# Optimization experiments

Hardware: AMD Instinct MI355X
Metric: run time of the kernel (lower is better)

The kernel has to match this reference:

```python
import jax, jax.numpy as jnp
import numpy as np
import math

L, HEADS, K, NFFN, H = 4, 8, 32, 2, 256  # layers, attention heads, top-k neighbors, FFN layers, hidden


def mish(x):
    return x * jnp.tanh(jax.nn.softplus(x))


def layernorm(x, a, b, eps=1e-6):
    # torch LayerNorm-style with UNBIASED std (x.std default), matching the source
    mean = x.mean(-1, keepdims=True)
    var = jnp.sum((x - mean) ** 2, axis=-1, keepdims=True) / (x.shape[-1] - 1)
    return a * (x - mean) / (jnp.sqrt(var) + eps) + b


def linear(x, W, b):
    # torch nn.Linear: y = x @ W^T + b, W is [out, in]
    return jnp.einsum('...i,oi->...o', x, W) + b


def setup_inputs() -> dict:
    key = jax.random.key(0)
    ks = jax.random.split(key, 6)
    node_features = jax.random.normal(ks[0], (16, 512, H), dtype=jnp.float32)
    edge_features = jax.random.uniform(ks[1], (16, 512, 512), dtype=jnp.float32)
    masks = jnp.ones((16, 512), dtype=jnp.int32)
    attn_W = jax.random.normal(ks[2], (L, 4, H, H), dtype=jnp.float32) * 0.05  # q,k,v,out per layer
    attn_b = jnp.zeros((L, 4, H), dtype=jnp.float32)
    ffn_W = jax.random.normal(ks[3], (L, NFFN, H, H), dtype=jnp.float32) * 0.05
    ffn_b = jnp.zeros((L, NFFN, H), dtype=jnp.float32)
    ln_a = jnp.ones((H,), dtype=jnp.float32)
    ln_b = jnp.zeros((H,), dtype=jnp.float32)
    return {"node_features": node_features, "edge_features": edge_features, "masks": masks,
            "attn_W": attn_W, "attn_b": attn_b, "ffn_W": ffn_W, "ffn_b": ffn_b,
            "ln_a": ln_a, "ln_b": ln_b}


def reference(node_features, edge_features, masks, attn_W, attn_b, ffn_W, ffn_b, ln_a, ln_b):
    b, m, _ = node_features.shape
    d = H // HEADS
    scale = 1.0 / math.sqrt(d)

    # top-k edge-weight mask (double argsort rank trick, as in source); deterministic
    rank = jnp.argsort(jnp.argsort(-edge_features, axis=-1), axis=-1)
    ew = edge_features * (rank < K)
    ew = ew / (jnp.sum(ew, axis=-1, keepdims=True) + 1e-5)  # [b, m, m]

    col_mask = (masks == 0)[:, None, None, :]  # broadcast over heads and query rows

    x = node_features
    for i in range(L):
        x = layernorm(x, ln_a, ln_b)
        # MHSA
        def split_heads(y):
            return y.reshape(b, m, HEADS, d).transpose(0, 2, 1, 3)  # b h m d
        q = split_heads(linear(x, attn_W[i, 0], attn_b[i, 0]))
        k = split_heads(linear(x, attn_W[i, 1], attn_b[i, 1]))
        v = split_heads(linear(x, attn_W[i, 2], attn_b[i, 2]))
        scores = jnp.einsum('bhmd,bhnd->bhmn', q, k)
        scores = jnp.where(col_mask, -1e12, scores)
        scores = jax.nn.softmax(scores * ew[:, None] * scale, axis=-1)
        attn_out = jnp.einsum('bhmn,bhnd->bhmd', scores, v)
        attn_out = attn_out.transpose(0, 2, 1, 3).reshape(b, m, H)
        attn_out = mish(linear(attn_out, attn_W[i, 3], attn_b[i, 3]))
        x = x + attn_out
        x = layernorm(x, ln_a, ln_b)
        # FFN: all layers use mish (output_act_fn='mish')
        y = x
        for j in range(NFFN):
            y = mish(linear(y, ffn_W[i, j], ffn_b[i, j]))
        x = x + y
    return x
```

## Files before the change

### kernel.cpp

```cpp
#include <hip/hip_runtime.h>
#include <cstddef>

#define NB 16
#define NM 512
#define NHID 256
#define NTOPK 32
#define NROWS (NB*NM)
#define NLAYER 4

typedef unsigned short ushort_t;
typedef __attribute__((ext_vector_type(8))) short short8;
typedef __attribute__((ext_vector_type(4))) short short4v;
typedef __attribute__((ext_vector_type(4))) float f32x4;

#define FRAG_OFF(row, c8) (((c8) >> 2) * 1024 + ((((c8) & 3) << 4) + (((row) & 15) ^ ((c8) >> 2))) * 16)
#define FRAG_RD(ks, lane) ((ks) * 1024 + ((((lane) >> 4) << 4) + (((lane) & 15) ^ (ks))) * 16)

#define MFMA16(a, b, c) __builtin_amdgcn_mfma_f32_16x16x32_bf16((a), (b), (c), 0, 0, 0)

__device__ __forceinline__ float mish_f(float v) {
    if (v > 20.0f) return v;
    float t = __expf(v);
    float u = t * (t + 2.0f);
    return v * (u / (u + 2.0f));
}
__device__ __forceinline__ ushort_t f2b(float f) {
    unsigned u = __float_as_uint(f);
    return (ushort_t)((u + 0x7FFFu + ((u >> 16) & 1u)) >> 16);
}
__device__ __forceinline__ float b2f(ushort_t h) {
    return __uint_as_float(((unsigned)h) << 16);
}

__global__ __launch_bounds__(256) void prep_kernel(const float* __restrict__ edge,
                                                   int* __restrict__ tidx,
                                                   float* __restrict__ tw,
                                                   const float* __restrict__ attnW,
                                                   const float* __restrict__ ffnW,
                                                   ushort_t* __restrict__ wb) {
    if (blockIdx.x < 768) {
        int t = blockIdx.x * 256 + threadIdx.x;
        int frag = t >> 9, r = t & 511;
        int ks = r >> 6, l = r & 63;
        const float* src;
        if (frag < 256) src = attnW + ((size_t)(frag >> 6) * 1024 + (frag & 63) * 16 + (l & 15)) * 256;
        else { int fi = frag - 256; src = ffnW + ((size_t)(fi >> 5) * 512 + (fi & 31) * 16 + (l & 15)) * 256; }
        src += ks * 32 + (l >> 4) * 8;
        short8 o;
        #pragma unroll
        for (int j = 0; j < 8; ++j) o[j] = (short)f2b(src[j]);
        *(short8*)(wb + (size_t)t * 8) = o;
        return;
    }
    const int lane = threadIdx.x & 63, w = threadIdx.x >> 6;
    const int row = (blockIdx.x - 768) * 4 + w;
    const float* er = edge + (size_t)row * NM;
    float v[8]; unsigned u[8];
    #pragma unroll
    for (int s = 0; s < 8; ++s) { v[s] = er[s * 64 + lane]; u[s] = __float_as_uint(v[s]); }
    unsigned T = 0;
    for (int bit = 31; bit >= 0; --bit) {
        unsigned Tc = T | (1u << bit);
        int c = 0;
        #pragma unroll
        for (int s = 0; s < 8; ++s) c += (int)__popcll(__ballot(u[s] >= Tc));
        if (c >= NTOPK) T = Tc;
    }
    int cgt = 0;
    #pragma unroll
    for (int s = 0; s < 8; ++s) cgt += (int)__popcll(__ballot(u[s] > T));
    const int extra = NTOPK - cgt;
    float psum = 0.f;
    #pragma unroll
    for (int s = 0; s < 8; ++s) psum += (u[s] > T) ? v[s] : 0.f;
    psum += __shfl_xor(psum, 1); psum += __shfl_xor(psum, 2); psum += __shfl_xor(psum, 4);
    psum += __shfl_xor(psum, 8); psum += __shfl_xor(psum, 16); psum += __shfl_xor(psum, 32);
    const float ssum = psum + (float)extra * __uint_as_float(T);
    const float rden = 0.17677669529663687f / (ssum + 1e-5f);
    const unsigned long long lmask = (1ull << lane) - 1ull;
    int base = 0, eqbase = 0;
    #pragma unroll
    for (int s = 0; s < 8; ++s) {
        bool gt = (u[s] > T), eq = (u[s] == T);
        unsigned long long meq = __ballot(eq);
        int eqrank = eqbase + (int)__popcll(meq & lmask);
        bool sel = gt || (eq && eqrank < extra);
        unsigned long long msel = __ballot(sel);
        if (sel) {
            int pos = base + (int)__popcll(msel & lmask);
            tidx[row * NTOPK + pos] = s * 64 + lane;
            tw[row * NTOPK + pos] = v[s] * rden;
        }
        base += (int)__popcll(msel);
        eqbase += (int)__popcll(meq);
    }
}

__global__ __launch_bounds__(256) void k1_ln_qkv(const float* __restrict__ xin,
                                                 float* __restrict__ x,
                                                 float* __restrict__ q,
                                                 ushort_t* __restrict__ kvb,
                                                 float* __restrict__ part,
                                                 const ushort_t* __restrict__ wf,
                                                 const float* __restrict__ bias,
                                                 const float* __restrict__ ga,
                                                 const float* __restrict__ gb) {
    __shared__ __align__(16) char af[8192];
    const int tid = threadIdx.x, lane = tid & 63, w = tid >> 6;
    const int bx = blockIdx.x;
    const int wid = (bx & 7) * 64 + (bx >> 3);
    const int bm = wid * 16, bb = wid >> 5, blk = wid & 31;
    const int zb = blockIdx.y;
    {
        const int rr = lane >> 4, c16 = (lane & 15) << 4;
        const int ri = (w << 2) + rr;
        const float* xr = xin + (size_t)(bm + ri) * NHID + c16;
        f32x4 v0 = *(const f32x4*)(xr);
        f32x4 v1 = *(const f32x4*)(xr + 4);
        f32x4 v2 = *(const f32x4*)(xr + 8);
        f32x4 v3 = *(const f32x4*)(xr + 12);
        float s = 0.f;
        #pragma unroll
        for (int k = 0; k < 4; ++k) s += v0[k] + v1[k] + v2[k] + v3[k];
        s += __shfl_xor(s, 1); s += __shfl_xor(s, 2); s += __shfl_xor(s, 4); s += __shfl_xor(s, 8);
        float mean = s * (1.0f / NHID);
        float vr = 0.f;
        #pragma unroll
        for (int k = 0; k < 4; ++k) {
            float d0 = v0[k]-mean, d1 = v1[k]-mean, d2 = v2[k]-mean, d3 = v3[k]-mean;
            vr += d0*d0 + d1*d1 + d2*d2 + d3*d3;
        }
        vr += __shfl_xor(vr, 1); vr += __shfl_xor(vr, 2); vr += __shfl_xor(vr, 4); vr += __shfl_xor(vr, 8);
        vr *= (1.0f / (NHID - 1));
        float rs = 1.0f / (sqrtf(vr) + 1e-6f);
        f32x4 g0 = *(const f32x4*)(ga + c16), g1 = *(const f32x4*)(ga + c16 + 4);
        f32x4 g2 = *(const f32x4*)(ga + c16 + 8), g3 = *(const f32x4*)(ga + c16 + 12);
        f32x4 h0 = *(const f32x4*)(gb + c16), h1 = *(const f32x4*)(gb + c16 + 4);
        f32x4 h2 = *(const f32x4*)(gb + c16 + 8), h3 = *(const f32x4*)(gb + c16 + 12);
        f32x4 o0, o1, o2, o3;
        #pragma unroll
        for (int k = 0; k < 4; ++k) {
            o0[k] = g0[k]*(v0[k]-mean)*rs + h0[k];
            o1[k] = g1[k]*(v1[k]-mean)*rs + h1[k];
            o2[k] = g2[k]*(v2[k]-mean)*rs + h2[k];
            o3[k] = g3[k]*(v3[k]-mean)*rs + h3[k];
        }
        if (zb == 0) {
            float* xw = x + (size_t)(bm + ri) * NHID + c16;
            *(f32x4*)(xw) = o0; *(f32x4*)(xw + 4) = o1;
            *(f32x4*)(xw + 8) = o2; *(f32x4*)(xw + 12) = o3;
        }
        short8 p0, p1;
        #pragma unroll
        for (int k = 0; k < 4; ++k) {
            p0[k] = (short)f2b(o0[k]); p0[4+k] = (short)f2b(o1[k]);
            p1[k] = (short)f2b(o2[k]); p1[4+k] = (short)f2b(o3[k]);
        }
        int c8 = (lane & 15) * 2;
        *(short8*)(af + FRAG_OFF(ri, c8)) = p0;
        *(short8*)(af + FRAG_OFF(ri, c8 + 1)) = p1;
    }
    __syncthreads();
    short8 a[8];
    #pragma unroll
    for (int ks = 0; ks < 8; ++ks) a[ks] = *(const short8*)(af + FRAG_RD(ks, lane));
    #pragma unroll
    for (int gi = 0; gi < 3; ++gi) {
        const int col0 = (zb * 3 + gi) * 128 + w * 32;
        f32x4 acc0 = {}, acc1 = {};
        const ushort_t* bp0 = wf + ((size_t)((col0 >> 4) * 8) * 64 + lane) * 8;
        const ushort_t* bp1 = bp0 + 4096;
        #pragma unroll
        for (int ks = 0; ks < 8; ++ks) {
            short8 b0 = *(const short8*)(bp0 + ks * 512);
            short8 b1 = *(const short8*)(bp1 + ks * 512);
            acc0 = MFMA16(a[ks], b0, acc0);
            acc1 = MFMA16(a[ks], b1, acc1);
        }
        const int rbase = bm + (lane >> 4) * 4;
        #pragma unroll
        for (int ni = 0; ni < 2; ++ni) {
            int col = col0 + ni * 16 + (lane & 15);
            float bv = bias[col];
            f32x4 A = ni ? acc1 : acc0;
            #pragma unroll
            for (int j = 0; j < 4; ++j) {
                int row = rbase + j;
                float vv = A[j] + bv;
                if (col < 256) q[(size_t)row * 256 + col] = vv;
                else kvb[(size_t)row * 512 + (col - 256)] = f2b(vv);
            }
            if (zb == 1 && gi >= 1) {
                float s2 = A[0] + A[1] + A[2] + A[3] + 4.0f * bv;
                s2 += __shfl_xor(s2, 16); s2 += __shfl_xor(s2, 32);
                if (lane < 16)
                    part[((size_t)bb * 32 + blk) * 256 + (col0 + ni * 16 + lane - 512)] = s2;
            }
        }
    }
}

template<int LAST>
__global__ __launch_bounds__(1024, 4) void kb_layer(float* __restrict__ x,
                                                    float* __restrict__ q,
                                                    const ushort_t* __restrict__ kvb_cur,
                                                    ushort_t* __restrict__ kvb_nxt,
                                                    const float* __restrict__ part_cur,
                                                    float* __restrict__ part_nxt,
                                                    const int* __restrict__ tidx,
                                                    const float* __restrict__ tw,
                                                    const int* __restrict__ msk,
                                                    const ushort_t* __restrict__ wfo,
                                                    const ushort_t* __restrict__ wf1,
                                                    const ushort_t* __restrict__ wf2,
                                                    const ushort_t* __restrict__ wqn,
                                                    const float* __restrict__ bo,
                                                    const float* __restrict__ b1,
                                                    const float* __restrict__ b2,
                                                    const float* __restrict__ bqn,
                                                    const float* __restrict__ ga,
                                                    const float* __restrict__ gb) {
    __shared__ __align__(16) float regA[32 * 256];
    __shared__ __align__(16) char regB[16384];
    __shared__ __align__(16) char regC[16384];
    const int tid = threadIdx.x, lane = tid & 63, w = tid >> 6;
    const int wid = (blockIdx.x & 7) * 32 + (blockIdx.x >> 3);
    const int R0 = wid * 32, bb = wid >> 4, blk = wid & 15;
    int* sidx = (int*)regC;
    float* sws = (float*)(regC + 4096);
    float* vsumf = regA;
    {
        int nb = tidx[(size_t)R0 * NTOPK + tid];
        float wv = tw[(size_t)R0 * NTOPK + tid];
        sidx[tid] = (msk[bb * NM + nb] == 0) ? (nb | (int)0x80000000) : nb;
        sws[tid] = wv;
    }
    if (tid < 256) {
        float s = 0.f;
        #pragma unroll
        for (int p = 0; p < 32; ++p) s += part_cur[((size_t)bb * 32 + p) * 256 + tid];
        vsumf[tid] = s;
    }
    float xres[2][4];
    #pragma unroll
    for (int rh = 0; rh < 2; ++rh)
        #pragma unroll
        for (int j = 0; j < 4; ++j)
            xres[rh][j] = x[(size_t)(R0 + rh * 16 + (lane >> 4) * 4 + j) * NHID + w * 16 + (lane & 15)];
    const int rl = w * 2 + (lane >> 5);
    const int cbase = (lane & 31) * 8;
    float qv[8];
    {
        const float* qp = q + (size_t)(R0 + rl) * 256 + cbase;
        f32x4 q0 = *(const f32x4*)qp, q1 = *(const f32x4*)(qp + 4);
        #pragma unroll
        for (int k = 0; k < 4; ++k) { qv[k] = q0[k]; qv[4 + k] = q1[k]; }
    }
    __syncthreads();
    {
        float accv[8] = {};
        float den = 0.f;
        for (int j = 0; j < NTOPK; ++j) {
            int raw = sidx[rl * 32 + j];
            float swv = sws[rl * 32 + j];
            const ushort_t* kp = kvb_cur + ((size_t)(bb * NM + (raw & 511))) * 512 + cbase;
            short8 kA = *(const short8*)(kp);
            short8 vA = *(const short8*)(kp + 256);
            float p = 0.f;
            #pragma unroll
            for (int t = 0; t < 8; ++t) p += qv[t] * b2f((ushort_t)kA[t]);
            p += __shfl_xor(p, 1); p += __shfl_xor(p, 2);
            float sarg = (raw < 0) ? -1e12f : p;
            float e = __expf(sarg * swv);
            float em1 = e - 1.0f;
            den += em1;
            #pragma unroll
            for (int t = 0; t < 8; ++t) accv[t] += em1 * b2f((ushort_t)vA[t]);
        }
        float rden = 1.0f / (den + 512.0f);
        short8 p0;
        #pragma unroll
        for (int t = 0; t < 8; ++t) p0[t] = (short)f2b((accv[t] + vsumf[cbase + t]) * rden);
        *(short8*)(regB + (rl >> 4) * 8192 + FRAG_OFF(rl, (lane & 31))) = p0;
    }
    __syncthreads();
    {
        short8 b[8];
        const ushort_t* bp = wfo + ((size_t)(w * 8) * 64 + lane) * 8;
        #pragma unroll
        for (int ks = 0; ks < 8; ++ks) b[ks] = *(const short8*)(bp + ks * 512);
        int col = w * 16 + (lane & 15);
        float bv = bo[col];
        #pragma unroll
        for (int rh = 0; rh < 2; ++rh) {
            f32x4 acc = {};
            #pragma unroll
            for (int ks = 0; ks < 8; ++ks)
                acc = MFMA16(*(const short8*)(regB + rh * 8192 + FRAG_RD(ks, lane)), b[ks], acc);
            #pragma unroll
            for (int j = 0; j < 4; ++j) {
                int row = rh * 16 + (lane >> 4) * 4 + j;
                regA[row * 256 + col] = mish_f(acc[j] + bv) + xres[rh][j];
            }
        }
    }
    __syncthreads();
    {
        const int c0 = (lane & 31) * 8;
        float* xr = regA + rl * 256 + c0;
        f32x4 v0 = *(const f32x4*)xr, v1 = *(const f32x4*)(xr + 4);
        float s = v0[0]+v0[1]+v0[2]+v0[3]+v1[0]+v1[1]+v1[2]+v1[3];
        s += __shfl_xor(s,1); s += __shfl_xor(s,2); s += __shfl_xor(s,4);
        s += __shfl_xor(s,8); s += __shfl_xor(s,16);
        float mean = s * (1.0f / NHID);
        float vr = 0.f;
        #pragma unroll
        for (int k = 0; k < 4; ++k) {
            float d0 = v0[k]-mean, d1 = v1[k]-mean;
            vr += d0*d0 + d1*d1;
        }
        vr += __shfl_xor(vr,1); vr += __shfl_xor(vr,2); vr += __shfl_xor(vr,4);
        vr += __shfl_xor(vr,8); vr += __shfl_xor(vr,16);
        vr *= (1.0f / (NHID - 1));
        float rs = 1.0f / (sqrtf(vr) + 1e-6f);
        f32x4 g0 = *(const f32x4*)(ga + c0), g1 = *(const f32x4*)(ga + c0 + 4);
        f32x4 h0 = *(const f32x4*)(gb + c0), h1 = *(const f32x4*)(gb + c0 + 4);
        f32x4 o0, o1;
        #pragma unroll
        for (int k = 0; k < 4; ++k) {
            o0[k] = g0[k]*(v0[k]-mean)*rs + h0[k];
            o1[k] = g1[k]*(v1[k]-mean)*rs + h1[k];
        }
        *(f32x4*)xr = o0; *(f32x4*)(xr + 4) = o1;
        short8 p;
        #pragma unroll
        for (int k = 0; k < 4; ++k) { p[k] = (short)f2b(o0[k]); p[4+k] = (short)f2b(o1[k]); }
        *(short8*)(regB + (rl >> 4) * 8192 + FRAG_OFF(rl, (lane & 31))) = p;
    }
    __syncthreads();
    {
        short8 b[8];
        const ushort_t* bp = wf1 + ((size_t)(w * 8) * 64 + lane) * 8;
        #pragma unroll
        for (int ks = 0; ks < 8; ++ks) b[ks] = *(const short8*)(bp + ks * 512);
        int col = w * 16 + (lane & 15);
        float bv = b1[col];
        int c8 = col >> 3;
        #pragma unroll
        for (int rh = 0; rh < 2; ++rh) {
            f32x4 acc = {};
            #pragma unroll
            for (int ks = 0; ks < 8; ++ks)
                acc = MFMA16(*(const short8*)(regB + rh * 8192 + FRAG_RD(ks, lane)), b[ks], acc);
            #pragma unroll
            for (int j = 0; j < 4; ++j) {
                int row = rh * 16 + (lane >> 4) * 4 + j;
                *(ushort_t*)(regC + rh * 8192 + FRAG_OFF(row, c8) + (col & 7) * 2) = f2b(mish_f(acc[j] + bv));
            }
        }
    }
    __syncthreads();
    {
        short8 b[8];
        const ushort_t* bp = wf2 + ((size_t)(w * 8) * 64 + lane) * 8;
        #pragma unroll
        for (int ks = 0; ks < 8; ++ks) b[ks] = *(const short8*)(bp + ks * 512);
        int col = w * 16 + (lane & 15);
        float bv = b2[col];
        #pragma unroll
        for (int rh = 0; rh < 2; ++rh) {
            f32x4 acc = {};
            #pragma unroll
            for (int ks = 0; ks < 8; ++ks)
                acc = MFMA16(*(const short8*)(regC + rh * 8192 + FRAG_RD(ks, lane)), b[ks], acc);
            #pragma unroll
            for (int j = 0; j < 4; ++j) {
                int row = rh * 16 + (lane >> 4) * 4 + j;
                float v = mish_f(acc[j] + bv) + regA[row * 256 + col];
                if (LAST) x[(size_t)(R0 + row) * NHID + col] = v;
                else regA[row * 256 + col] = v;
            }
        }
    }
    if (LAST) return;
    __syncthreads();
    {
        const int c0 = (lane & 31) * 8;
        float* xr = regA + rl * 256 + c0;
        f32x4 v0 = *(const f32x4*)xr, v1 = *(const f32x4*)(xr + 4);
        float s = v0[0]+v0[1]+v0[2]+v0[3]+v1[0]+v1[1]+v1[2]+v1[3];
        s += __shfl_xor(s,1); s += __shfl_xor(s,2); s += __shfl_xor(s,4);
        s += __shfl_xor(s,8); s += __shfl_xor(s,16);
        float mean = s * (1.0f / NHID);
        float vr = 0.f;
        #pragma unroll
        for (int k = 0; k < 4; ++k) {
            float d0 = v0[k]-mean, d1 = v1[k]-mean;
            vr += d0*d0 + d1*d1;
        }
        vr += __shfl_xor(vr,1); vr += __shfl_xor(vr,2); vr += __shfl_xor(vr,4);
        vr += __shfl_xor(vr,8); vr += __shfl_xor(vr,16);
        vr *= (1.0f / (NHID - 1));
        float rs = 1.0f / (sqrtf(vr) + 1e-6f);
        f32x4 g0 = *(const f32x4*)(ga + c0), g1 = *(const f32x4*)(ga + c0 + 4);
        f32x4 h0 = *(const f32x4*)(gb + c0), h1 = *(const f32x4*)(gb + c0 + 4);
        f32x4 o0, o1;
        #pragma unroll
        for (int k = 0; k < 4; ++k) {
            o0[k] = g0[k]*(v0[k]-mean)*rs + h0[k];
            o1[k] = g1[k]*(v1[k]-mean)*rs + h1[k];
        }
        float* xg = x + (size_t)(R0 + rl) * NHID + c0;
        *(f32x4*)xg = o0; *(f32x4*)(xg + 4) = o1;
        short8 p;
        #pragma unroll
        for (int k = 0; k < 4; ++k) { p[k] = (short)f2b(o0[k]); p[4+k] = (short)f2b(o1[k]); }
        *(short8*)(regB + (rl >> 4) * 8192 + FRAG_OFF(rl, (lane & 31))) = p;
    }
    __syncthreads();
    {
        #pragma unroll
        for (int gg = 0; gg < 3; ++gg) {
            const int ct = w + gg * 16;
            short8 b[8];
            const ushort_t* bp = wqn + (size_t)ct * 4096 + (size_t)lane * 8;
            #pragma unroll
            for (int ks = 0; ks < 8; ++ks) b[ks] = *(const short8*)(bp + ks * 512);
            int col = ct * 16 + (lane & 15);
            float bv = bqn[col];
            #pragma unroll
            for (int rh = 0; rh < 2; ++rh) {
                f32x4 acc = {};
                #pragma unroll
                for (int ks = 0; ks < 8; ++ks)
                    acc = MFMA16(*(const short8*)(regB + rh * 8192 + FRAG_RD(ks, lane)), b[ks], acc);
                #pragma unroll
                for (int j = 0; j < 4; ++j) {
                    int row = rh * 16 + (lane >> 4) * 4 + j;
                    float vv = acc[j] + bv;
                    if (col < 256) q[(size_t)(R0 + row) * 256 + col] = vv;
                    else kvb_nxt[(size_t)(R0 + row) * 512 + (col - 256)] = f2b(vv);
                }
                if (gg == 2) {
                    float s2 = acc[0] + acc[1] + acc[2] + acc[3] + 4.0f * bv;
                    s2 += __shfl_xor(s2, 16); s2 += __shfl_xor(s2, 32);
                    if (lane < 16)
                        part_nxt[((size_t)bb * 32 + blk * 2 + rh) * 256 + (ct * 16 + lane - 512)] = s2;
                }
            }
        }
    }
}

extern "C" void kernel_launch(void* const* d_in, const int* in_sizes, int n_in,
                              void* d_out, int out_size, void* d_ws, size_t ws_size,
                              hipStream_t stream) {
    (void)in_sizes; (void)n_in; (void)out_size; (void)ws_size;
    const float* node  = (const float*)d_in[0];
    const float* edge  = (const float*)d_in[1];
    const int*   msk   = (const int*)d_in[2];
    const float* attnW = (const float*)d_in[3];
    const float* attnB = (const float*)d_in[4];
    const float* ffnW  = (const float*)d_in[5];
    const float* ffnB  = (const float*)d_in[6];
    const float* lna   = (const float*)d_in[7];
    const float* lnb   = (const float*)d_in[8];

    float* x = (float*)d_out;
    float* wsf = (float*)d_ws;
    float*    q     = wsf;
    ushort_t* kvbA  = (ushort_t*)(wsf + 2097152);
    ushort_t* kvbB  = (ushort_t*)(wsf + 4194304);
    ushort_t* wb    = (ushort_t*)(wsf + 6291456);
    float*    tw    = wsf + 7077888;
    int*      tidx  = (int*)(wsf + 7340032);
    float*    partA = wsf + 7602176;
    float*    partB = wsf + 7733248;

    prep_kernel<<<2816, 256, 0, stream>>>(edge, tidx, tw, attnW, ffnW, wb);
    k1_ln_qkv<<<dim3(512, 2), 256, 0, stream>>>(node, x, q, kvbA, partA,
                                                wb, attnB, lna, lnb);
    for (int l = 0; l < NLAYER; ++l) {
        ushort_t* kv_c = (l & 1) ? kvbB : kvbA;
        ushort_t* kv_n = (l & 1) ? kvbA : kvbB;
        float* pt_c = (l & 1) ? partB : partA;
        float* pt_n = (l & 1) ? partA : partB;
        const ushort_t* wfo = wb + (size_t)(l * 64 + 48) * 4096;
        const ushort_t* wf1 = wb + (size_t)(256 + l * 32) * 4096;
        const ushort_t* wf2 = wb + (size_t)(256 + l * 32 + 16) * 4096;
        const ushort_t* wqn = wb + (size_t)(((l + 1) & 3) * 64) * 4096;
        const float* bo  = attnB + (size_t)l * 1024 + 768;
        const float* b1  = ffnB + (size_t)l * 512;
        const float* b2  = b1 + 256;
        const float* bqn = attnB + (size_t)((l + 1) & 3) * 1024;
        if (l < NLAYER - 1)
            kb_layer<0><<<256, 1024, 0, stream>>>(x, q, kv_c, kv_n, pt_c, pt_n,
                tidx, tw, msk, wfo, wf1, wf2, wqn, bo, b1, b2, bqn, lna, lnb);
        else
            kb_layer<1><<<256, 1024, 0, stream>>>(x, q, kv_c, kv_n, pt_c, pt_n,
                tidx, tw, msk, wfo, wf1, wf2, wqn, bo, b1, b2, bqn, lna, lnb);
    }
}
```

Before: 168.3 us.

## Fuse LN/QKV and all layers into one cooperative persistent kernel

Replaces the separate LN+QKV kernel and the four per-layer launches with a single cooperative kernel that loops over layers and separates them with grid-wide syncs. Q and the residual x now stay in LDS (padded stride) across layers instead of round-tripping through global memory. This removes launch overhead and some global traffic, but adds the cost of grid.sync and more LDS per block, which may lower occupancy.

```diff
diff --git a/kernel.cpp b/kernel.cpp
--- a/kernel.cpp
+++ b/kernel.cpp
@@ -1,5 +1,8 @@
 #include <hip/hip_runtime.h>
+#include <hip/hip_cooperative_groups.h>
 #include <cstddef>
+
+namespace cg = cooperative_groups;
 
 #define NB 16
 #define NM 512
@@ -7,10 +10,10 @@
 #define NTOPK 32
 #define NROWS (NB*NM)
 #define NLAYER 4
+#define XP 260
 
 typedef unsigned short ushort_t;
 typedef __attribute__((ext_vector_type(8))) short short8;
-typedef __attribute__((ext_vector_type(4))) short short4v;
 typedef __attribute__((ext_vector_type(4))) float f32x4;
 
 #define FRAG_OFF(row, c8) (((c8) >> 2) * 1024 + ((((c8) & 3) << 4) + (((row) & 15) ^ ((c8) >> 2))) * 16)
@@ -96,218 +99,42 @@
     }
 }
 
-__global__ __launch_bounds__(256) void k1_ln_qkv(const float* __restrict__ xin,
-                                                 float* __restrict__ x,
-                                                 float* __restrict__ q,
-                                                 ushort_t* __restrict__ kvb,
-                                                 float* __restrict__ part,
-                                                 const ushort_t* __restrict__ wf,
-                                                 const float* __restrict__ bias,
-                                                 const float* __restrict__ ga,
-                                                 const float* __restrict__ gb) {
-    __shared__ __align__(16) char af[8192];
-    const int tid = threadIdx.x, lane = tid & 63, w = tid >> 6;
-    const int bx = blockIdx.x;
-    const int wid = (bx & 7) * 64 + (bx >> 3);
-    const int bm = wid * 16, bb = wid >> 5, blk = wid & 31;
-    const int zb = blockIdx.y;
-    {
-        const int rr = lane >> 4, c16 = (lane & 15) << 4;
-        const int ri = (w << 2) + rr;
-        const float* xr = xin + (size_t)(bm + ri) * NHID + c16;
-        f32x4 v0 = *(const f32x4*)(xr);
-        f32x4 v1 = *(const f32x4*)(xr + 4);
-        f32x4 v2 = *(const f32x4*)(xr + 8);
-        f32x4 v3 = *(const f32x4*)(xr + 12);
-        float s = 0.f;
-        #pragma unroll
-        for (int k = 0; k < 4; ++k) s += v0[k] + v1[k] + v2[k] + v3[k];
-        s += __shfl_xor(s, 1); s += __shfl_xor(s, 2); s += __shfl_xor(s, 4); s += __shfl_xor(s, 8);
-        float mean = s * (1.0f / NHID);
-        float vr = 0.f;
-        #pragma unroll
-        for (int k = 0; k < 4; ++k) {
-            float d0 = v0[k]-mean, d1 = v1[k]-mean, d2 = v2[k]-mean, d3 = v3[k]-mean;
-            vr += d0*d0 + d1*d1 + d2*d2 + d3*d3;
-        }
-        vr += __shfl_xor(vr, 1); vr += __shfl_xor(vr, 2); vr += __shfl_xor(vr, 4); vr += __shfl_xor(vr, 8);
-        vr *= (1.0f / (NHID - 1));
-        float rs = 1.0f / (sqrtf(vr) + 1e-6f);
-        f32x4 g0 = *(const f32x4*)(ga + c16), g1 = *(const f32x4*)(ga + c16 + 4);
-        f32x4 g2 = *(const f32x4*)(ga + c16 + 8), g3 = *(const f32x4*)(ga + c16 + 12);
-        f32x4 h0 = *(const f32x4*)(gb + c16), h1 = *(const f32x4*)(gb + c16 + 4);
-        f32x4 h2 = *(const f32x4*)(gb + c16 + 8), h3 = *(const f32x4*)(gb + c16 + 12);
-        f32x4 o0, o1, o2, o3;
-        #pragma unroll
-        for (int k = 0; k < 4; ++k) {
-            o0[k] = g0[k]*(v0[k]-mean)*rs + h0[k];
-            o1[k] = g1[k]*(v1[k]-mean)*rs + h1[k];
-            o2[k] = g2[k]*(v2[k]-mean)*rs + h2[k];
-            o3[k] = g3[k]*(v3[k]-mean)*rs + h3[k];
-        }
-        if (zb == 0) {
-            float* xw = x + (size_t)(bm + ri) * NHID + c16;
-            *(f32x4*)(xw) = o0; *(f32x4*)(xw + 4) = o1;
-            *(f32x4*)(xw + 8) = o2; *(f32x4*)(xw + 12) = o3;
-        }
-        short8 p0, p1;
-        #pragma unroll
-        for (int k = 0; k < 4; ++k) {
-            p0[k] = (short)f2b(o0[k]); p0[4+k] = (short)f2b(o1[k]);
-            p1[k] = (short)f2b(o2[k]); p1[4+k] = (short)f2b(o3[k]);
-        }
-        int c8 = (lane & 15) * 2;
-        *(short8*)(af + FRAG_OFF(ri, c8)) = p0;
-        *(short8*)(af + FRAG_OFF(ri, c8 + 1)) = p1;
-    }
-    __syncthreads();
-    short8 a[8];
-    #pragma unroll
-    for (int ks = 0; ks < 8; ++ks) a[ks] = *(const short8*)(af + FRAG_RD(ks, lane));
-    #pragma unroll
-    for (int gi = 0; gi < 3; ++gi) {
-        const int col0 = (zb * 3 + gi) * 128 + w * 32;
-        f32x4 acc0 = {}, acc1 = {};
-        const ushort_t* bp0 = wf + ((size_t)((col0 >> 4) * 8) * 64 + lane) * 8;
-        const ushort_t* bp1 = bp0 + 4096;
-        #pragma unroll
-        for (int ks = 0; ks < 8; ++ks) {
-            short8 b0 = *(const short8*)(bp0 + ks * 512);
-            short8 b1 = *(const short8*)(bp1 + ks * 512);
-            acc0 = MFMA16(a[ks], b0, acc0);
-            acc1 = MFMA16(a[ks], b1, acc1);
-        }
-        const int rbase = bm + (lane >> 4) * 4;
-        #pragma unroll
-        for (int ni = 0; ni < 2; ++ni) {
-            int col = col0 + ni * 16 + (lane & 15);
-            float bv = bias[col];
-            f32x4 A = ni ? acc1 : acc0;
-            #pragma unroll
-            for (int j = 0; j < 4; ++j) {
-                int row = rbase + j;
-                float vv = A[j] + bv;
-                if (col < 256) q[(size_t)row * 256 + col] = vv;
-                else kvb[(size_t)row * 512 + (col - 256)] = f2b(vv);
-            }
-            if (zb == 1 && gi >= 1) {
-                float s2 = A[0] + A[1] + A[2] + A[3] + 4.0f * bv;
-                s2 += __shfl_xor(s2, 16); s2 += __shfl_xor(s2, 32);
-                if (lane < 16)
-                    part[((size_t)bb * 32 + blk) * 256 + (col0 + ni * 16 + lane - 512)] = s2;
-            }
-        }
-    }
-}
-
-template<int LAST>
-__global__ __launch_bounds__(1024, 4) void kb_layer(float* __restrict__ x,
-                                                    float* __restrict__ q,
-                                                    const ushort_t* __restrict__ kvb_cur,
-                                                    ushort_t* __restrict__ kvb_nxt,
-                                                    const float* __restrict__ part_cur,
-                                                    float* __restrict__ part_nxt,
-                                                    const int* __restrict__ tidx,
-                                                    const float* __restrict__ tw,
-                                                    const int* __restrict__ msk,
-                                                    const ushort_t* __restrict__ wfo,
-                                                    const ushort_t* __restrict__ wf1,
-                                                    const ushort_t* __restrict__ wf2,
-                                                    const ushort_t* __restrict__ wqn,
-                                                    const float* __restrict__ bo,
-                                                    const float* __restrict__ b1,
-                                                    const float* __restrict__ b2,
-                                                    const float* __restrict__ bqn,
-                                                    const float* __restrict__ ga,
-                                                    const float* __restrict__ gb) {
-    __shared__ __align__(16) float regA[32 * 256];
+__global__ __launch_bounds__(1024, 4) void mk_kernel(float* __restrict__ x,
+                                                     const float* __restrict__ node,
+                                                     ushort_t* __restrict__ kvbA,
+                                                     ushort_t* __restrict__ kvbB,
+                                                     float* __restrict__ partA,
+                                                     float* __restrict__ partB,
+                                                     const int* __restrict__ tidx,
+                                                     const float* __restrict__ tw,
+                                                     const int* __restrict__ msk,
+                                                     const ushort_t* __restrict__ wb,
+                                                     const float* __restrict__ attnB,
+                                                     const float* __restrict__ ffnB,
+                                                     const float* __restrict__ lna,
+                                                     const float* __restrict__ lnb) {
+    __shared__ __align__(16) float regA[32 * XP];
+    __shared__ __align__(16) float qlds[32 * XP];
     __shared__ __align__(16) char regB[16384];
     __shared__ __align__(16) char regC[16384];
+    __shared__ int sidxL[1024];
+    __shared__ float swsL[1024];
+    __shared__ float vsumf[256];
+    cg::grid_group grid = cg::this_grid();
     const int tid = threadIdx.x, lane = tid & 63, w = tid >> 6;
     const int wid = (blockIdx.x & 7) * 32 + (blockIdx.x >> 3);
     const int R0 = wid * 32, bb = wid >> 4, blk = wid & 15;
-    int* sidx = (int*)regC;
-    float* sws = (float*)(regC + 4096);
-    float* vsumf = regA;
+    const int rl = w * 2 + (lane >> 5);
+    const int c0 = (lane & 31) * 8;
+
     {
         int nb = tidx[(size_t)R0 * NTOPK + tid];
         float wv = tw[(size_t)R0 * NTOPK + tid];
-        sidx[tid] = (msk[bb * NM + nb] == 0) ? (nb | (int)0x80000000) : nb;
-        sws[tid] = wv;
-    }
-    if (tid < 256) {
-        float s = 0.f;
-        #pragma unroll
-        for (int p = 0; p < 32; ++p) s += part_cur[((size_t)bb * 32 + p) * 256 + tid];
-        vsumf[tid] = s;
-    }
-    float xres[2][4];
-    #pragma unroll
-    for (int rh = 0; rh < 2; ++rh)
-        #pragma unroll
-        for (int j = 0; j < 4; ++j)
-            xres[rh][j] = x[(size_t)(R0 + rh * 16 + (lane >> 4) * 4 + j) * NHID + w * 16 + (lane & 15)];
-    const int rl = w * 2 + (lane >> 5);
-    const int cbase = (lane & 31) * 8;
-    float qv[8];
+        sidxL[tid] = (msk[bb * NM + nb] == 0) ? (nb | (int)0x80000000) : nb;
+        swsL[tid] = wv;
+    }
     {
-        const float* qp = q + (size_t)(R0 + rl) * 256 + cbase;
-        f32x4 q0 = *(const f32x4*)qp, q1 = *(const f32x4*)(qp + 4);
-        #pragma unroll
-        for (int k = 0; k < 4; ++k) { qv[k] = q0[k]; qv[4 + k] = q1[k]; }
-    }
-    __syncthreads();
-    {
-        float accv[8] = {};
-        float den = 0.f;
-        for (int j = 0; j < NTOPK; ++j) {
-            int raw = sidx[rl * 32 + j];
-            float swv = sws[rl * 32 + j];
-            const ushort_t* kp = kvb_cur + ((size_t)(bb * NM + (raw & 511))) * 512 + cbase;
-            short8 kA = *(const short8*)(kp);
-            short8 vA = *(const short8*)(kp + 256);
-            float p = 0.f;
-            #pragma unroll
-            for (int t = 0; t < 8; ++t) p += qv[t] * b2f((ushort_t)kA[t]);
-            p += __shfl_xor(p, 1); p += __shfl_xor(p, 2);
-            float sarg = (raw < 0) ? -1e12f : p;
-            float e = __expf(sarg * swv);
-            float em1 = e - 1.0f;
-            den += em1;
-            #pragma unroll
-            for (int t = 0; t < 8; ++t) accv[t] += em1 * b2f((ushort_t)vA[t]);
-        }
-        float rden = 1.0f / (den + 512.0f);
-        short8 p0;
-        #pragma unroll
-        for (int t = 0; t < 8; ++t) p0[t] = (short)f2b((accv[t] + vsumf[cbase + t]) * rden);
-        *(short8*)(regB + (rl >> 4) * 8192 + FRAG_OFF(rl, (lane & 31))) = p0;
-    }
-    __syncthreads();
-    {
-        short8 b[8];
-        const ushort_t* bp = wfo + ((size_t)(w * 8) * 64 + lane) * 8;
-        #pragma unroll
-        for (int ks = 0; ks < 8; ++ks) b[ks] = *(const short8*)(bp + ks * 512);
-        int col = w * 16 + (lane & 15);
-        float bv = bo[col];
-        #pragma unroll
-        for (int rh = 0; rh < 2; ++rh) {
-            f32x4 acc = {};
-            #pragma unroll
-            for (int ks = 0; ks < 8; ++ks)
-                acc = MFMA16(*(const short8*)(regB + rh * 8192 + FRAG_RD(ks, lane)), b[ks], acc);
-            #pragma unroll
-            for (int j = 0; j < 4; ++j) {
-                int row = rh * 16 + (lane >> 4) * 4 + j;
-                regA[row * 256 + col] = mish_f(acc[j] + bv) + xres[rh][j];
-            }
-        }
-    }
-    __syncthreads();
-    {
-        const int c0 = (lane & 31) * 8;
-        float* xr = regA + rl * 256 + c0;
+        const float* xr = node + (size_t)(R0 + rl) * NHID + c0;
         f32x4 v0 = *(const f32x4*)xr, v1 = *(const f32x4*)(xr + 4);
         float s = v0[0]+v0[1]+v0[2]+v0[3]+v1[0]+v1[1]+v1[2]+v1[3];
         s += __shfl_xor(s,1); s += __shfl_xor(s,2); s += __shfl_xor(s,4);
@@ -323,15 +150,16 @@
         vr += __shfl_xor(vr,8); vr += __shfl_xor(vr,16);
         vr *= (1.0f / (NHID - 1));
         float rs = 1.0f / (sqrtf(vr) + 1e-6f);
-        f32x4 g0 = *(const f32x4*)(ga + c0), g1 = *(const f32x4*)(ga + c0 + 4);
-        f32x4 h0 = *(const f32x4*)(gb + c0), h1 = *(const f32x4*)(gb + c0 + 4);
+        f32x4 g0 = *(const f32x4*)(lna + c0), g1 = *(const f32x4*)(lna + c0 + 4);
+        f32x4 h0 = *(const f32x4*)(lnb + c0), h1 = *(const f32x4*)(lnb + c0 + 4);
         f32x4 o0, o1;
         #pragma unroll
         for (int k = 0; k < 4; ++k) {
             o0[k] = g0[k]*(v0[k]-mean)*rs + h0[k];
             o1[k] = g1[k]*(v1[k]-mean)*rs + h1[k];
         }
-        *(f32x4*)xr = o0; *(f32x4*)(xr + 4) = o1;
+        float* ar = regA + rl * XP + c0;
+        *(f32x4*)ar = o0; *(f32x4*)(ar + 4) = o1;
         short8 p;
         #pragma unroll
         for (int k = 0; k < 4; ++k) { p[k] = (short)f2b(o0[k]); p[4+k] = (short)f2b(o1[k]); }
@@ -339,95 +167,17 @@
     }
     __syncthreads();
     {
-        short8 b[8];
-        const ushort_t* bp = wf1 + ((size_t)(w * 8) * 64 + lane) * 8;
-        #pragma unroll
-        for (int ks = 0; ks < 8; ++ks) b[ks] = *(const short8*)(bp + ks * 512);
-        int col = w * 16 + (lane & 15);
-        float bv = b1[col];
-        int c8 = col >> 3;
-        #pragma unroll
-        for (int rh = 0; rh < 2; ++rh) {
-            f32x4 acc = {};
-            #pragma unroll
-            for (int ks = 0; ks < 8; ++ks)
-                acc = MFMA16(*(const short8*)(regB + rh * 8192 + FRAG_RD(ks, lane)), b[ks], acc);
-            #pragma unroll
-            for (int j = 0; j < 4; ++j) {
-                int row = rh * 16 + (lane >> 4) * 4 + j;
-                *(ushort_t*)(regC + rh * 8192 + FRAG_OFF(row, c8) + (col & 7) * 2) = f2b(mish_f(acc[j] + bv));
-            }
-        }
-    }
-    __syncthreads();
-    {
-        short8 b[8];
-        const ushort_t* bp = wf2 + ((size_t)(w * 8) * 64 + lane) * 8;
-        #pragma unroll
-        for (int ks = 0; ks < 8; ++ks) b[ks] = *(const short8*)(bp + ks * 512);
-        int col = w * 16 + (lane & 15);
-        float bv = b2[col];
-        #pragma unroll
-        for (int rh = 0; rh < 2; ++rh) {
-            f32x4 acc = {};
-            #pragma unroll
-            for (int ks = 0; ks < 8; ++ks)
-                acc = MFMA16(*(const short8*)(regC + rh * 8192 + FRAG_RD(ks, lane)), b[ks], acc);
-            #pragma unroll
-            for (int j = 0; j < 4; ++j) {
-                int row = rh * 16 + (lane >> 4) * 4 + j;
-                float v = mish_f(acc[j] + bv) + regA[row * 256 + col];
-                if (LAST) x[(size_t)(R0 + row) * NHID + col] = v;
-                else regA[row * 256 + col] = v;
-            }
-        }
-    }
-    if (LAST) return;
-    __syncthreads();
-    {
-        const int c0 = (lane & 31) * 8;
-        float* xr = regA + rl * 256 + c0;
-        f32x4 v0 = *(const f32x4*)xr, v1 = *(const f32x4*)(xr + 4);
-        float s = v0[0]+v0[1]+v0[2]+v0[3]+v1[0]+v1[1]+v1[2]+v1[3];
-        s += __shfl_xor(s,1); s += __shfl_xor(s,2); s += __shfl_xor(s,4);
-        s += __shfl_xor(s,8); s += __shfl_xor(s,16);
-        float mean = s * (1.0f / NHID);
-        float vr = 0.f;
-        #pragma unroll
-        for (int k = 0; k < 4; ++k) {
-            float d0 = v0[k]-mean, d1 = v1[k]-mean;
-            vr += d0*d0 + d1*d1;
-        }
-        vr += __shfl_xor(vr,1); vr += __shfl_xor(vr,2); vr += __shfl_xor(vr,4);
-        vr += __shfl_xor(vr,8); vr += __shfl_xor(vr,16);
-        vr *= (1.0f / (NHID - 1));
-        float rs = 1.0f / (sqrtf(vr) + 1e-6f);
-        f32x4 g0 = *(const f32x4*)(ga + c0), g1 = *(const f32x4*)(ga + c0 + 4);
-        f32x4 h0 = *(const f32x4*)(gb + c0), h1 = *(const f32x4*)(gb + c0 + 4);
-        f32x4 o0, o1;
-        #pragma unroll
-        for (int k = 0; k < 4; ++k) {
-            o0[k] = g0[k]*(v0[k]-mean)*rs + h0[k];
-            o1[k] = g1[k]*(v1[k]-mean)*rs + h1[k];
-        }
-        float* xg = x + (size_t)(R0 + rl) * NHID + c0;
-        *(f32x4*)xg = o0; *(f32x4*)(xg + 4) = o1;
-        short8 p;
-        #pragma unroll
-        for (int k = 0; k < 4; ++k) { p[k] = (short)f2b(o0[k]); p[4+k] = (short)f2b(o1[k]); }
-        *(short8*)(regB + (rl >> 4) * 8192 + FRAG_OFF(rl, (lane & 31))) = p;
-    }
-    __syncthreads();
-    {
+        const ushort_t* wq = wb;
+        const float* bq = attnB;
         #pragma unroll
         for (int gg = 0; gg < 3; ++gg) {
             const int ct = w + gg * 16;
             short8 b[8];
-            const ushort_t* bp = wqn + (size_t)ct * 4096 + (size_t)lane * 8;
+            const ushort_t* bp = wq + (size_t)ct * 4096 + (size_t)lane * 8;
             #pragma unroll
             for (int ks = 0; ks < 8; ++ks) b[ks] = *(const short8*)(bp + ks * 512);
             int col = ct * 16 + (lane & 15);
-            float bv = bqn[col];
+            float bv = bq[col];
             #pragma unroll
             for (int rh = 0; rh < 2; ++rh) {
                 f32x4 acc = {};
@@ -438,17 +188,238 @@
                 for (int j = 0; j < 4; ++j) {
                     int row = rh * 16 + (lane >> 4) * 4 + j;
                     float vv = acc[j] + bv;
-                    if (col < 256) q[(size_t)(R0 + row) * 256 + col] = vv;
-                    else kvb_nxt[(size_t)(R0 + row) * 512 + (col - 256)] = f2b(vv);
+                    if (col < 256) qlds[row * XP + col] = vv;
+                    else kvbA[(size_t)(R0 + row) * 512 + (col - 256)] = f2b(vv);
                 }
                 if (gg == 2) {
                     float s2 = acc[0] + acc[1] + acc[2] + acc[3] + 4.0f * bv;
                     s2 += __shfl_xor(s2, 16); s2 += __shfl_xor(s2, 32);
                     if (lane < 16)
-                        part_nxt[((size_t)bb * 32 + blk * 2 + rh) * 256 + (ct * 16 + lane - 512)] = s2;
-                }
-            }
-        }
+                        partA[((size_t)bb * 32 + blk * 2 + rh) * 256 + (ct * 16 + lane - 512)] = s2;
+                }
+            }
+        }
+    }
+    grid.sync();
+
+    ushort_t* kv_c = kvbA; ushort_t* kv_n = kvbB;
+    float* pt_c = partA; float* pt_n = partB;
+    for (int l = 0; l < NLAYER; ++l) {
+        const ushort_t* wfo = wb + (size_t)(l * 64 + 48) * 4096;
+        const ushort_t* wf1 = wb + (size_t)(256 + l * 32) * 4096;
+        const ushort_t* wf2 = wb + (size_t)(256 + l * 32 + 16) * 4096;
+        const float* bo = attnB + (size_t)l * 1024 + 768;
+        const float* b1 = ffnB + (size_t)l * 512;
+        const float* b2 = b1 + 256;
+        if (tid < 256) {
+            float s = 0.f;
+            #pragma unroll
+            for (int p = 0; p < 32; ++p) s += pt_c[((size_t)bb * 32 + p) * 256 + tid];
+            vsumf[tid] = s;
+        }
+        {
+            float qv[8];
+            {
+                const float* qp = qlds + rl * XP + c0;
+                f32x4 q0 = *(const f32x4*)qp, q1 = *(const f32x4*)(qp + 4);
+                #pragma unroll
+                for (int k = 0; k < 4; ++k) { qv[k] = q0[k]; qv[4 + k] = q1[k]; }
+            }
+            float accv[8] = {};
+            float den = 0.f;
+            for (int j = 0; j < NTOPK; ++j) {
+                int raw = sidxL[rl * 32 + j];
+                float swv = swsL[rl * 32 + j];
+                const ushort_t* kp = kv_c + ((size_t)(bb * NM + (raw & 511))) * 512 + c0;
+                short8 kA = *(const short8*)(kp);
+                short8 vA = *(const short8*)(kp + 256);
+                float p = 0.f;
+                #pragma unroll
+                for (int t = 0; t < 8; ++t) p += qv[t] * b2f((ushort_t)kA[t]);
+                p += __shfl_xor(p, 1); p += __shfl_xor(p, 2);
+                float sarg = (raw < 0) ? -1e12f : p;
+                float e = __expf(sarg * swv);
+                float em1 = e - 1.0f;
+                den += em1;
+                #pragma unroll
+                for (int t = 0; t < 8; ++t) accv[t] += em1 * b2f((ushort_t)vA[t]);
+            }
+            __syncthreads();
+            float rden = 1.0f / (den + 512.0f);
+            short8 p0;
+            #pragma unroll
+            for (int t = 0; t < 8; ++t) p0[t] = (short)f2b((accv[t] + vsumf[c0 + t]) * rden);
+            *(short8*)(regB + (rl >> 4) * 8192 + FRAG_OFF(rl, (lane & 31))) = p0;
+        }
+        __syncthreads();
+        {
+            short8 b[8];
+            const ushort_t* bp = wfo + ((size_t)(w * 8) * 64 + lane) * 8;
+            #pragma unroll
+            for (int ks = 0; ks < 8; ++ks) b[ks] = *(const short8*)(bp + ks * 512);
+            int col = w * 16 + (lane & 15);
+            float bv = bo[col];
+            #pragma unroll
+            for (int rh = 0; rh < 2; ++rh) {
+                f32x4 acc = {};
+                #pragma unroll
+                for (int ks = 0; ks < 8; ++ks)
+                    acc = MFMA16(*(const short8*)(regB + rh * 8192 + FRAG_RD(ks, lane)), b[ks], acc);
+                #pragma unroll
+                for (int j = 0; j < 4; ++j) {
+                    int row = rh * 16 + (lane >> 4) * 4 + j;
+                    regA[row * XP + col] = mish_f(acc[j] + bv) + regA[row * XP + col];
+                }
+            }
+        }
+        __syncthreads();
+        {
+            float* xr = regA + rl * XP + c0;
+            f32x4 v0 = *(const f32x4*)xr, v1 = *(const f32x4*)(xr + 4);
+            float s = v0[0]+v0[1]+v0[2]+v0[3]+v1[0]+v1[1]+v1[2]+v1[3];
+            s += __shfl_xor(s,1); s += __shfl_xor(s,2); s += __shfl_xor(s,4);
+            s += __shfl_xor(s,8); s += __shfl_xor(s,16);
+            float mean = s * (1.0f / NHID);
+            float vr = 0.f;
+            #pragma unroll
+            for (int k = 0; k < 4; ++k) {
+                float d0 = v0[k]-mean, d1 = v1[k]-mean;
+                vr += d0*d0 + d1*d1;
+            }
+            vr += __shfl_xor(vr,1); vr += __shfl_xor(vr,2); vr += __shfl_xor(vr,4);
+            vr += __shfl_xor(vr,8); vr += __shfl_xor(vr,16);
+            vr *= (1.0f / (NHID - 1));
+            float rs = 1.0f / (sqrtf(vr) + 1e-6f);
+            f32x4 g0 = *(const f32x4*)(lna + c0), g1 = *(const f32x4*)(lna + c0 + 4);
+            f32x4 h0 = *(const f32x4*)(lnb + c0), h1 = *(const f32x4*)(lnb + c0 + 4);
+            f32x4 o0, o1;
+            #pragma unroll
+            for (int k = 0; k < 4; ++k) {
+                o0[k] = g0[k]*(v0[k]-mean)*rs + h0[k];
+                o1[k] = g1[k]*(v1[k]-mean)*rs + h1[k];
+            }
+            *(f32x4*)xr = o0; *(f32x4*)(xr + 4) = o1;
+            short8 p;
+            #pragma unroll
+            for (int k = 0; k < 4; ++k) { p[k] = (short)f2b(o0[k]); p[4+k] = (short)f2b(o1[k]); }
+            *(short8*)(regB + (rl >> 4) * 8192 + FRAG_OFF(rl, (lane & 31))) = p;
+        }
+        __syncthreads();
+        {
+            short8 b[8];
+            const ushort_t* bp = wf1 + ((size_t)(w * 8) * 64 + lane) * 8;
+            #pragma unroll
+            for (int ks = 0; ks < 8; ++ks) b[ks] = *(const short8*)(bp + ks * 512);
+            int col = w * 16 + (lane & 15);
+            float bv = b1[col];
+            int c8 = col >> 3;
+            #pragma unroll
+            for (int rh = 0; rh < 2; ++rh) {
+                f32x4 acc = {};
+                #pragma unroll
+                for (int ks = 0; ks < 8; ++ks)
+                    acc = MFMA16(*(const short8*)(regB + rh * 8192 + FRAG_RD(ks, lane)), b[ks], acc);
+                #pragma unroll
+                for (int j = 0; j < 4; ++j) {
+                    int row = rh * 16 + (lane >> 4) * 4 + j;
+                    *(ushort_t*)(regC + rh * 8192 + FRAG_OFF(row, c8) + (col & 7) * 2) = f2b(mish_f(acc[j] + bv));
+                }
+            }
+        }
+        __syncthreads();
+        {
+            short8 b[8];
+            const ushort_t* bp = wf2 + ((size_t)(w * 8) * 64 + lane) * 8;
+            #pragma unroll
+            for (int ks = 0; ks < 8; ++ks) b[ks] = *(const short8*)(bp + ks * 512);
+            int col = w * 16 + (lane & 15);
+            float bv = b2[col];
+            #pragma unroll
+            for (int rh = 0; rh < 2; ++rh) {
+                f32x4 acc = {};
+                #pragma unroll
+                for (int ks = 0; ks < 8; ++ks)
+                    acc = MFMA16(*(const short8*)(regC + rh * 8192 + FRAG_RD(ks, lane)), b[ks], acc);
+                #pragma unroll
+                for (int j = 0; j < 4; ++j) {
+                    int row = rh * 16 + (lane >> 4) * 4 + j;
+                    float v = mish_f(acc[j] + bv) + regA[row * XP + col];
+                    if (l == NLAYER - 1) x[(size_t)(R0 + row) * NHID + col] = v;
+                    else regA[row * XP + col] = v;
+                }
+            }
+        }
+        if (l == NLAYER - 1) return;
+        __syncthreads();
+        {
+            float* xr = regA + rl * XP + c0;
+            f32x4 v0 = *(const f32x4*)xr, v1 = *(const f32x4*)(xr + 4);
+            float s = v0[0]+v0[1]+v0[2]+v0[3]+v1[0]+v1[1]+v1[2]+v1[3];
+            s += __shfl_xor(s,1); s += __shfl_xor(s,2); s += __shfl_xor(s,4);
+            s += __shfl_xor(s,8); s += __shfl_xor(s,16);
+            float mean = s * (1.0f / NHID);
+            float vr = 0.f;
+            #pragma unroll
+            for (int k = 0; k < 4; ++k) {
+                float d0 = v0[k]-mean, d1 = v1[k]-mean;
+                vr += d0*d0 + d1*d1;
+            }
+            vr += __shfl_xor(vr,1); vr += __shfl_xor(vr,2); vr += __shfl_xor(vr,4);
+            vr += __shfl_xor(vr,8); vr += __shfl_xor(vr,16);
+            vr *= (1.0f / (NHID - 1));
+            float rs = 1.0f / (sqrtf(vr) + 1e-6f);
+            f32x4 g0 = *(const f32x4*)(lna + c0), g1 = *(const f32x4*)(lna + c0 + 4);
+            f32x4 h0 = *(const f32x4*)(lnb + c0), h1 = *(const f32x4*)(lnb + c0 + 4);
+            f32x4 o0, o1;
+            #pragma unroll
+            for (int k = 0; k < 4; ++k) {
+                o0[k] = g0[k]*(v0[k]-mean)*rs + h0[k];
+                o1[k] = g1[k]*(v1[k]-mean)*rs + h1[k];
+            }
+            *(f32x4*)xr = o0; *(f32x4*)(xr + 4) = o1;
+            short8 p;
+            #pragma unroll
+            for (int k = 0; k < 4; ++k) { p[k] = (short)f2b(o0[k]); p[4+k] = (short)f2b(o1[k]); }
+            *(short8*)(regB + (rl >> 4) * 8192 + FRAG_OFF(rl, (lane & 31))) = p;
+        }
+        __syncthreads();
+        {
+            const ushort_t* wqn = wb + (size_t)((l + 1) * 64) * 4096;
+            const float* bqn = attnB + (size_t)(l + 1) * 1024;
+            #pragma unroll
+            for (int gg = 0; gg < 3; ++gg) {
+                const int ct = w + gg * 16;
+                short8 b[8];
+                const ushort_t* bp = wqn + (size_t)ct * 4096 + (size_t)lane * 8;
+                #pragma unroll
+                for (int ks = 0; ks < 8; ++ks) b[ks] = *(const short8*)(bp + ks * 512);
+                int col = ct * 16 + (lane & 15);
+                float bv = bqn[col];
+                #pragma unroll
+                for (int rh = 0; rh < 2; ++rh) {
+                    f32x4 acc = {};
+                    #pragma unroll
+                    for (int ks = 0; ks < 8; ++ks)
+                        acc = MFMA16(*(const short8*)(regB + rh * 8192 + FRAG_RD(ks, lane)), b[ks], acc);
+                    #pragma unroll
+                    for (int j = 0; j < 4; ++j) {
+                        int row = rh * 16 + (lane >> 4) * 4 + j;
+                        float vv = acc[j] + bv;
+                        if (col < 256) qlds[row * XP + col] = vv;
+                        else kv_n[(size_t)(R0 + row) * 512 + (col - 256)] = f2b(vv);
+                    }
+                    if (gg == 2) {
+                        float s2 = acc[0] + acc[1] + acc[2] + acc[3] + 4.0f * bv;
+                        s2 += __shfl_xor(s2, 16); s2 += __shfl_xor(s2, 32);
+                        if (lane < 16)
+                            pt_n[((size_t)bb * 32 + blk * 2 + rh) * 256 + (ct * 16 + lane - 512)] = s2;
+                    }
+                }
+            }
+        }
+        grid.sync();
+        ushort_t* kt = kv_c; kv_c = kv_n; kv_n = kt;
+        float* pt = pt_c; pt_c = pt_n; pt_n = pt;
     }
 }
 
@@ -468,36 +439,20 @@
 
     float* x = (float*)d_out;
     float* wsf = (float*)d_ws;
-    float*    q     = wsf;
-    ushort_t* kvbA  = (ushort_t*)(wsf + 2097152);
-    ushort_t* kvbB  = (ushort_t*)(wsf + 4194304);
-    ushort_t* wb    = (ushort_t*)(wsf + 6291456);
-    float*    tw    = wsf + 7077888;
-    int*      tidx  = (int*)(wsf + 7340032);
-    float*    partA = wsf + 7602176;
-    float*    partB = wsf + 7733248;
+    ushort_t* kvbA  = (ushort_t*)wsf;
+    ushort_t* kvbB  = (ushort_t*)(wsf + 2097152);
+    ushort_t* wb    = (ushort_t*)(wsf + 4194304);
+    float*    tw    = wsf + 4980736;
+    int*      tidx  = (int*)(wsf + 5242880);
+    float*    partA = wsf + 5505024;
+    float*    partB = wsf + 5636096;
 
     prep_kernel<<<2816, 256, 0, stream>>>(edge, tidx, tw, attnW, ffnW, wb);
-    k1_ln_qkv<<<dim3(512, 2), 256, 0, stream>>>(node, x, q, kvbA, partA,
-                                                wb, attnB, lna, lnb);
-    for (int l = 0; l < NLAYER; ++l) {
-        ushort_t* kv_c = (l & 1) ? kvbB : kvbA;
-        ushort_t* kv_n = (l & 1) ? kvbA : kvbB;
-        float* pt_c = (l & 1) ? partB : partA;
-        float* pt_n = (l & 1) ? partA : partB;
-        const ushort_t* wfo = wb + (size_t)(l * 64 + 48) * 4096;
-        const ushort_t* wf1 = wb + (size_t)(256 + l * 32) * 4096;
-        const ushort_t* wf2 = wb + (size_t)(256 + l * 32 + 16) * 4096;
-        const ushort_t* wqn = wb + (size_t)(((l + 1) & 3) * 64) * 4096;
-        const float* bo  = attnB + (size_t)l * 1024 + 768;
-        const float* b1  = ffnB + (size_t)l * 512;
-        const float* b2  = b1 + 256;
-        const float* bqn = attnB + (size_t)((l + 1) & 3) * 1024;
-        if (l < NLAYER - 1)
-            kb_layer<0><<<256, 1024, 0, stream>>>(x, q, kv_c, kv_n, pt_c, pt_n,
-                tidx, tw, msk, wfo, wf1, wf2, wqn, bo, b1, b2, bqn, lna, lnb);
-        else
-            kb_layer<1><<<256, 1024, 0, stream>>>(x, q, kv_c, kv_n, pt_c, pt_n,
-                tidx, tw, msk, wfo, wf1, wf2, wqn, bo, b1, b2, bqn, lna, lnb);
-    }
-}
+
+    void* kargs[] = { (void*)&x, (void*)&node, (void*)&kvbA, (void*)&kvbB,
+                      (void*)&partA, (void*)&partB, (void*)&tidx, (void*)&tw,
+                      (void*)&msk, (void*)&wb, (void*)&attnB, (void*)&ffnB,
+                      (void*)&lna, (void*)&lnb };
+    hipLaunchCooperativeKernel((void*)mk_kernel, dim3(256), dim3(1024),
+                               kargs, 0, stream);
+}
```

Measured after the change: 328.6 us. 1.95x slower.
